# Performance work log

Measured on AMD Instinct MI355X. Metric: run time of the kernel, lower is better.

## Reference

```python
import jax, jax.numpy as jnp
import numpy as np

D_MODEL = 512
NUM_HEADS = 8
HEAD_DIM = D_MODEL // NUM_HEADS
ATTN_WINDOW = 256


def setup_inputs() -> dict:
    key = jax.random.key(0)
    ks = jax.random.split(key, 5)
    B, S = 2, 4096
    x = jax.random.normal(ks[0], (B, S, D_MODEL), dtype=jnp.float32)
    s = 1.0 / np.sqrt(D_MODEL)
    qkv_w = jax.random.uniform(ks[1], (3 * D_MODEL, D_MODEL), minval=-s, maxval=s, dtype=jnp.float32)
    qkv_b = jax.random.uniform(ks[2], (3 * D_MODEL,), minval=-s, maxval=s, dtype=jnp.float32)
    out_w = jax.random.uniform(ks[3], (D_MODEL, D_MODEL), minval=-s, maxval=s, dtype=jnp.float32)
    out_b = jax.random.uniform(ks[4], (D_MODEL,), minval=-s, maxval=s, dtype=jnp.float32)
    return {"x": x, "qkv_w": qkv_w, "qkv_b": qkv_b, "out_w": out_w, "out_b": out_b}


def reference(x, qkv_w, qkv_b, out_w, out_b):
    B, S, D = x.shape
    scale = HEAD_DIM ** (-0.5)
    qkv = x @ qkv_w.T + qkv_b                       # [B,S,3D]
    qkv = qkv.reshape(B, S, 3, NUM_HEADS, HEAD_DIM)
    q, k, v = qkv[:, :, 0], qkv[:, :, 1], qkv[:, :, 2]
    scores = jnp.einsum('bthd,bshd->bhts', q, k) * scale  # [B,H,S,S]
    i = jnp.arange(S)[:, None]
    j = jnp.arange(S)[None, :]
    # causal AND within sliding window of size ATTN_WINDOW
    mask = (j <= i) & (j >= i - ATTN_WINDOW)        # [S,S] bool
    scores = jnp.where(mask, scores, -jnp.inf)
    weights = jax.nn.softmax(scores, axis=-1)
    out = jnp.einsum('bhts,bshd->bthd', weights, v).reshape(B, S, D)
    return out @ out_w.T + out_b
```

## Files before the change

kernel.cpp:

```cpp
#include <hip/hip_runtime.h>

#define S_LEN 4096
#define BATCH 2
#define DM 512
#define NH 8
#define DH 64
#define WINDOW 256

typedef __bf16 bf16x8 __attribute__((ext_vector_type(8)));
typedef float f32x4 __attribute__((ext_vector_type(4)));

typedef const __attribute__((address_space(1))) unsigned int* gas_ptr;
typedef __attribute__((address_space(3))) unsigned int* las_ptr;

#define SCALE_LOG2E 0.1803368801111204f
#define FIXED_MAX 16.0f

#define BAR()                                   \
  do {                                          \
    asm volatile("" ::: "memory");              \
    __builtin_amdgcn_s_barrier();               \
    asm volatile("" ::: "memory");              \
  } while (0)
#define WAITVM(N) asm volatile("s_waitcnt vmcnt(" #N ")" ::: "memory")

__device__ __forceinline__ unsigned short b16(float f) {
  __bf16 h = (__bf16)f;
  return __builtin_bit_cast(unsigned short, h);
}

#define N4_X (8192 * 512 / 4)
#define N4_QW (1536 * 512 / 4)
#define N4_OW (512 * 512 / 4)
__global__ __launch_bounds__(256) void convert_all(const float* __restrict__ x,
                                                   const float* __restrict__ qw,
                                                   const float* __restrict__ ow,
                                                   unsigned short* __restrict__ dst) {
  const int i = blockIdx.x * blockDim.x + threadIdx.x;
  const float4* src;
  int off;
  if (i < N4_X) { src = (const float4*)x; off = 0; }
  else if (i < N4_X + N4_QW) { src = (const float4*)qw; off = N4_X; }
  else { src = (const float4*)ow; off = N4_X + N4_QW; }
  const float4 v = src[i - off];
  ushort4 o;
  o.x = b16(v.x); o.y = b16(v.y); o.z = b16(v.z); o.w = b16(v.w);
  ((ushort4*)dst)[i] = o;
}


__device__ __forceinline__ void gemm_core(const unsigned short* __restrict__ A,
                                          const unsigned short* __restrict__ Bm,
                                          int m0, int n0,
                                          unsigned short* sA, unsigned short* sB,
                                          f32x4 acc[4][4]) {
  const int t = threadIdx.x;
  const int wave = t >> 6, lane = t & 63;
  const int wr = wave >> 1, wc = wave & 1;
  const int quad = lane >> 4, l16 = lane & 15;
  const int sw2 = (l16 >> 1) & 3;
  const int cq = (quad ^ sw2) * 8;

#define QKV_STAGE(k0, buf)                                                       \
  do {                                                                           \
    _Pragma("unroll") for (int p = 0; p < 2; ++p) {                              \
      const int ci = wave * 128 + p * 64 + lane;               \
      const int row = ci >> 2;                                                   \
      const int cg = (ci & 3) ^ ((ci >> 3) & 3);  \
      const unsigned short* ga = A + (size_t)(m0 + row) * 512 + (k0) + cg * 8;   \
      __builtin_amdgcn_global_load_lds(                                          \
          (gas_ptr)(const void*)ga,                                              \
          (las_ptr)(void*)(sA + (buf) * 4096 + wave * 1024 + p * 512), 16, 0, 0);\
      const unsigned short* gb = Bm + (size_t)(n0 + row) * 512 + (k0) + cg * 8;  \
      __builtin_amdgcn_global_load_lds(                                          \
          (gas_ptr)(const void*)gb,                                              \
          (las_ptr)(void*)(sB + (buf) * 4096 + wave * 1024 + p * 512), 16, 0, 0);\
    }                                                                            \
  } while (0)

  QKV_STAGE(0, 0);
  for (int k0 = 0; k0 < 512; k0 += 32) {
    const int cur = (k0 >> 5) & 1;
    BAR();
    if (k0 + 32 < 512) {
      QKV_STAGE(k0 + 32, cur ^ 1);
      WAITVM(4);
    } else {
      WAITVM(0);
    }
    BAR();
    const unsigned short* bA = sA + cur * 4096;
    const unsigned short* bB = sB + cur * 4096;
    bf16x8 af[4], bff[4];
#pragma unroll
    for (int i = 0; i < 4; ++i)
      af[i] = *(const bf16x8*)&bA[(wr * 64 + i * 16 + l16) * 32 + cq];
#pragma unroll
    for (int j = 0; j < 4; ++j)
      bff[j] = *(const bf16x8*)&bB[(wc * 64 + j * 16 + l16) * 32 + cq];
#pragma unroll
    for (int i = 0; i < 4; ++i)
#pragma unroll
      for (int j = 0; j < 4; ++j)
        acc[i][j] = __builtin_amdgcn_mfma_f32_16x16x32_bf16(af[i], bff[j], acc[i][j], 0, 0, 0);
  }
#undef QKV_STAGE
}

__global__ __launch_bounds__(256, 4) void gemm_qkv(const unsigned short* __restrict__ xb,
                                                   const unsigned short* __restrict__ wb,
                                                   const float* __restrict__ bias,
                                                   unsigned short* __restrict__ Qb,
                                                   unsigned short* __restrict__ Kb,
                                                   unsigned short* __restrict__ Vt) {
  __shared__ __align__(16) unsigned short sA[2 * 128 * 32];
  __shared__ __align__(16) unsigned short sB[2 * 128 * 32];
  f32x4 acc[4][4] = {};
  const int id = blockIdx.x;
  const int X = id & 7;
  const int t2 = id >> 3;
  const int cb = t2 % 12;
  const int rb = (t2 / 12) * 8 + X;
  const int m0 = rb * 128, n0 = cb * 128;
  gemm_core(xb, wb, m0, n0, sA, sB, acc);

  const int t = threadIdx.x;
  const int wave = t >> 6, lane = t & 63;
  const int wr = wave >> 1, wc = wave & 1;
  const int quad = lane >> 4, l16 = lane & 15;
#pragma unroll
  for (int j = 0; j < 4; ++j) {
    const int n = n0 + wc * 64 + j * 16 + l16;
    const float bv = bias[n];
#pragma unroll
    for (int i = 0; i < 4; ++i) {
      const int mr = m0 + wr * 64 + i * 16 + quad * 4;
      if (n < DM) {
#pragma unroll
        for (int r = 0; r < 4; ++r)
          Qb[(size_t)(mr + r) * DM + n] = b16((acc[i][j][r] + bv) * SCALE_LOG2E);
      } else if (n < 2 * DM) {
#pragma unroll
        for (int r = 0; r < 4; ++r)
          Kb[(size_t)(mr + r) * DM + (n - DM)] = b16(acc[i][j][r] + bv);
      } else {
        const int d = n & 63, h = (n - 2 * DM) >> 6;
#pragma unroll
        for (int r = 0; r < 4; ++r) {
          const int m = mr + r;
          const int b = m >> 12, s = m & (S_LEN - 1);
          Vt[((size_t)((b * NH + h) * DH + d)) * S_LEN + s] = b16(acc[i][j][r] + bv);
        }
      }
    }
  }
}

__global__ __launch_bounds__(256) void gemm_out(const unsigned short* __restrict__ Ab,
                                                const unsigned short* __restrict__ wb,
                                                const float* __restrict__ bias,
                                                float* __restrict__ C) {
  __shared__ __align__(16) unsigned short sA[2 * 64 * 32];
  __shared__ __align__(16) unsigned short sB[2 * 128 * 32];
  const int t = threadIdx.x;
  const int wave = t >> 6, lane = t & 63;
  const int wr = wave >> 1, wc = wave & 1;
  const int quad = lane >> 4, l16 = lane & 15;
  const int sw2 = (l16 >> 1) & 3;
  const int cq = (quad ^ sw2) * 8;
  const int id = blockIdx.x;
  const int X = id & 7;
  const int t2 = id >> 3;
  const int cb = t2 % 4;
  const int rb = (t2 / 4) * 8 + X;
  const int m0 = rb * 64, n0 = cb * 128;

#define OUT_STAGE(k0, buf)                                                       \
  do {                                                                           \
    {                                                                            \
      const int row = t >> 2;                                                    \
      const int cg = (t & 3) ^ ((t >> 3) & 3);                                   \
      const unsigned short* ga = Ab + (size_t)(m0 + row) * 512 + (k0) + cg * 8;  \
      __builtin_amdgcn_global_load_lds(                                          \
          (gas_ptr)(const void*)ga,                                              \
          (las_ptr)(void*)(sA + (buf) * 2048 + wave * 512), 16, 0, 0);           \
    }                                                                            \
    _Pragma("unroll") for (int p = 0; p < 2; ++p) {                              \
      const int ci = wave * 128 + p * 64 + lane;                                 \
      const int row = ci >> 2;                                                   \
      const int cg = (ci & 3) ^ ((ci >> 3) & 3);                                 \
      const unsigned short* gb = wb + (size_t)(n0 + row) * 512 + (k0) + cg * 8;  \
      __builtin_amdgcn_global_load_lds(                                          \
          (gas_ptr)(const void*)gb,                                              \
          (las_ptr)(void*)(sB + (buf) * 4096 + wave * 1024 + p * 512), 16, 0, 0);\
    }                                                                            \
  } while (0)

  f32x4 acc[2][4] = {};
  OUT_STAGE(0, 0);
  for (int k0 = 0; k0 < 512; k0 += 32) {
    const int cur = (k0 >> 5) & 1;
    BAR();
    if (k0 + 32 < 512) {
      OUT_STAGE(k0 + 32, cur ^ 1);
      WAITVM(3);
    } else {
      WAITVM(0);
    }
    BAR();
    const unsigned short* bA = sA + cur * 2048;
    const unsigned short* bB = sB + cur * 4096;
    bf16x8 af[2], bff[4];
#pragma unroll
    for (int i = 0; i < 2; ++i)
      af[i] = *(const bf16x8*)&bA[(wr * 32 + i * 16 + l16) * 32 + cq];
#pragma unroll
    for (int j = 0; j < 4; ++j)
      bff[j] = *(const bf16x8*)&bB[(wc * 64 + j * 16 + l16) * 32 + cq];
#pragma unroll
    for (int i = 0; i < 2; ++i)
#pragma unroll
      for (int j = 0; j < 4; ++j)
        acc[i][j] = __builtin_amdgcn_mfma_f32_16x16x32_bf16(af[i], bff[j], acc[i][j], 0, 0, 0);
  }
#undef OUT_STAGE

#pragma unroll
  for (int j = 0; j < 4; ++j) {
    const int n = n0 + wc * 64 + j * 16 + l16;
    const float bv = bias[n];
#pragma unroll
    for (int i = 0; i < 2; ++i) {
      const int mr = m0 + wr * 32 + i * 16 + quad * 4;
#pragma unroll
      for (int r = 0; r < 4; ++r)
        C[(size_t)(mr + r) * DM + n] = acc[i][j][r] + bv;
    }
  }
}

__global__ __launch_bounds__(256) void attn_mfma(const unsigned short* __restrict__ Qb,
                                                 const unsigned short* __restrict__ Kb,
                                                 const unsigned short* __restrict__ Vt,
                                                 unsigned short* __restrict__ AO) {
  __shared__ __align__(16) unsigned short Ks[2 * 64 * 64];
  __shared__ __align__(16) unsigned short Vs[2 * 64 * 64];
  __shared__ __align__(16) unsigned short Ps[64 * 64];
  const int t = threadIdx.x;
  const int wave = t >> 6, lane = t & 63;
  const int quad = lane >> 4, l16 = lane & 15;

  const int id = blockIdx.x;
  const int X = id & 7;
  const int o = (id >> 3) & 7;
  const int h = (id >> 6) & 7;
  const int b = id >> 9;
  const int g = (X - h) & 7;
  const int qt = g * 8 + o;
  const int q0 = qt * 64;

  const unsigned short* Kbase = Kb + (size_t)b * S_LEN * DM + h * DH;
  const unsigned short* Vbase = Vt + (size_t)((b * NH + h) * DH) * S_LEN;

  const unsigned short* qrow =
      Qb + (size_t)(b * S_LEN + q0 + wave * 16 + l16) * DM + h * DH;
  const bf16x8 aq0 = *(const bf16x8*)(qrow + quad * 8);
  const bf16x8 aq1 = *(const bf16x8*)(qrow + 32 + quad * 8);

  const int first = (qt >= 4) ? 0 : (4 - qt);

  int grow[2], gcol[2];
#pragma unroll
  for (int s = 0; s < 2; ++s) {
    const int L = t + 256 * s;
    grow[s] = L >> 3;
    gcol[s] = ((L & 7) ^ (grow[s] & 7)) * 8;
  }

#define ATTN_STAGE(c0, buf)                                                       \
  do {                                                                            \
    _Pragma("unroll") for (int s = 0; s < 2; ++s) {                               \
      const unsigned short* gk = Kbase + (size_t)((c0) + grow[s]) * DM + gcol[s]; \
      __builtin_amdgcn_global_load_lds(                                           \
          (gas_ptr)(const void*)gk,                                               \
          (las_ptr)(void*)(Ks + (buf) * 4096 + wave * 512 + s * 2048), 16, 0, 0); \
      const unsigned short* gv = Vbase + (size_t)grow[s] * S_LEN + (c0) + gcol[s];\
      __builtin_amdgcn_global_load_lds(                                           \
          (gas_ptr)(const void*)gv,                                               \
          (las_ptr)(void*)(Vs + (buf) * 4096 + wave * 512 + s * 2048), 16, 0, 0); \
    }                                                                             \
  } while (0)

  ATTN_STAGE(q0 - WINDOW + first * 64, first & 1);

  float l_ = 0.f;
  f32x4 O[4] = {};

  const int sw = l16 & 7;
  const int c0q = (quad ^ sw) * 8;
  const int c1q = ((quad | 4) ^ sw) * 8;

#pragma unroll
  for (int c = 0; c < 5; ++c) {
    if (c < first) continue;
    const int c0 = q0 - WINDOW + c * 64;
    const int cur = c & 1;
    BAR();
    if (c < 4) {
      ATTN_STAGE(c0 + 64, cur ^ 1);
      WAITVM(4);
    } else {
      WAITVM(0);
    }
    BAR();

    const unsigned short* Kc = Ks + cur * 4096;
    const unsigned short* Vc = Vs + cur * 4096;

    f32x4 sc[4];
#pragma unroll
    for (int nt = 0; nt < 4; ++nt) {
      const int krow = (nt * 16 + l16) * 64;
      bf16x8 bk0 = *(const bf16x8*)&Kc[krow + c0q];
      bf16x8 bk1 = *(const bf16x8*)&Kc[krow + c1q];
      f32x4 z = {};
      z = __builtin_amdgcn_mfma_f32_16x16x32_bf16(bk0, aq0, z, 0, 0, 0);
      sc[nt] = __builtin_amdgcn_mfma_f32_16x16x32_bf16(bk1, aq1, z, 0, 0, 0);
    }

    const int iiq = wave * 16 + l16;
    const int prow = iiq * 64;
#pragma unroll
    for (int nt = 0; nt < 4; ++nt) {
#pragma unroll
      for (int r = 0; r < 4; ++r) {
        const int jjk = nt * 16 + quad * 4 + r;
        float p = exp2f(sc[nt][r] - FIXED_MAX);
        if (c == 0) p = (jjk >= iiq) ? p : 0.f;
        if (c == 4) p = (jjk <= iiq) ? p : 0.f;
        sc[nt][r] = p;
        l_ += p;
      }
      ushort4 pk;
      pk.x = b16(sc[nt][0]);
      pk.y = b16(sc[nt][1]);
      pk.z = b16(sc[nt][2]);
      pk.w = b16(sc[nt][3]);
      *(ushort4*)&Ps[prow + (((nt * 2 + (quad >> 1)) ^ sw) * 8) + (quad & 1) * 4] = pk;
    }

    const bf16x8 bp0 = *(const bf16x8*)&Ps[prow + c0q];
    const bf16x8 bp1 = *(const bf16x8*)&Ps[prow + c1q];

#pragma unroll
    for (int nt = 0; nt < 4; ++nt) {
      const int vrow = (nt * 16 + l16) * 64;
      bf16x8 bv0 = *(const bf16x8*)&Vc[vrow + c0q];
      bf16x8 bv1 = *(const bf16x8*)&Vc[vrow + c1q];
      O[nt] = __builtin_amdgcn_mfma_f32_16x16x32_bf16(bv0, bp0, O[nt], 0, 0, 0);
      O[nt] = __builtin_amdgcn_mfma_f32_16x16x32_bf16(bv1, bp1, O[nt], 0, 0, 0);
    }
  }
#undef ATTN_STAGE

  l_ += __shfl_xor(l_, 16);
  l_ += __shfl_xor(l_, 32);
  const float linv = 1.f / l_;

  unsigned short* aoRow =
      AO + (size_t)(b * S_LEN + q0 + wave * 16 + l16) * DM + h * DH;
#pragma unroll
  for (int nt = 0; nt < 4; ++nt) {
    ushort4 o4;
    o4.x = b16(O[nt][0] * linv);
    o4.y = b16(O[nt][1] * linv);
    o4.z = b16(O[nt][2] * linv);
    o4.w = b16(O[nt][3] * linv);
    *(ushort4*)(aoRow + nt * 16 + quad * 4) = o4;
  }
}

extern "C" void kernel_launch(void* const* d_in, const int* in_sizes, int n_in,
                              void* d_out, int out_size, void* d_ws, size_t ws_size,
                              hipStream_t stream) {
  const float* x = (const float*)d_in[0];
  const float* qkv_w = (const float*)d_in[1];
  const float* qkv_b = (const float*)d_in[2];
  const float* out_w = (const float*)d_in[3];
  const float* out_b = (const float*)d_in[4];
  float* out = (float*)d_out;

  const int M = BATCH * S_LEN;
  unsigned short* ws = (unsigned short*)d_ws;
  unsigned short* xb   = ws;
  unsigned short* wqkv = xb + (size_t)M * DM;
  unsigned short* wout = wqkv + 3 * DM * DM;
  unsigned short* Qb   = wout + DM * DM;
  unsigned short* Kb   = Qb + (size_t)M * DM;
  unsigned short* Vt   = Kb + (size_t)M * DM;
  unsigned short* AO   = Vt + (size_t)M * DM;

  convert_all<<<(N4_X + N4_QW + N4_OW) / 256, 256, 0, stream>>>(x, qkv_w, out_w, xb);

  gemm_qkv<<<768, 256, 0, stream>>>(xb, wqkv, qkv_b, Qb, Kb, Vt);

  attn_mfma<<<1024, 256, 0, stream>>>(Qb, Kb, Vt, AO);

  gemm_out<<<512, 256, 0, stream>>>(AO, wout, out_b, out);
}
```

Baseline: 127.7 us.

## Fuse fp32-to-bf16 conversion into GEMM staging, drop separate convert kernel

Removes the standalone conversion kernel and has the QKV and output GEMMs load fp32 inputs and weights into registers, convert them to bf16 and write them into swizzled LDS, with a register-prefetch double buffer. This saves one launch and the write and re-read of the bf16 copies of x and the weights. In exchange, each GEMM block now reads fp32 (twice the bytes) and re-converts the weights many times across tiles. Direct global-to-LDS loads are replaced by register staging, which adds VGPR pressure, and the launch-bounds occupancy hint on gemm_qkv is dropped.

```diff
diff --git a/kernel.cpp b/kernel.cpp
--- a/kernel.cpp
+++ b/kernel.cpp
@@ -9,6 +9,7 @@
 
 typedef __bf16 bf16x8 __attribute__((ext_vector_type(8)));
 typedef float f32x4 __attribute__((ext_vector_type(4)));
+typedef unsigned short u16x8 __attribute__((ext_vector_type(8)));
 
 typedef const __attribute__((address_space(1))) unsigned int* gas_ptr;
 typedef __attribute__((address_space(3))) unsigned int* las_ptr;
@@ -23,96 +24,27 @@
     asm volatile("" ::: "memory");              \
   } while (0)
 #define WAITVM(N) asm volatile("s_waitcnt vmcnt(" #N ")" ::: "memory")
+#define WAITLGKM(N) asm volatile("s_waitcnt lgkmcnt(" #N ")" ::: "memory")
 
 __device__ __forceinline__ unsigned short b16(float f) {
   __bf16 h = (__bf16)f;
   return __builtin_bit_cast(unsigned short, h);
 }
 
-#define N4_X (8192 * 512 / 4)
-#define N4_QW (1536 * 512 / 4)
-#define N4_OW (512 * 512 / 4)
-__global__ __launch_bounds__(256) void convert_all(const float* __restrict__ x,
-                                                   const float* __restrict__ qw,
-                                                   const float* __restrict__ ow,
-                                                   unsigned short* __restrict__ dst) {
-  const int i = blockIdx.x * blockDim.x + threadIdx.x;
-  const float4* src;
-  int off;
-  if (i < N4_X) { src = (const float4*)x; off = 0; }
-  else if (i < N4_X + N4_QW) { src = (const float4*)qw; off = N4_X; }
-  else { src = (const float4*)ow; off = N4_X + N4_QW; }
-  const float4 v = src[i - off];
-  ushort4 o;
-  o.x = b16(v.x); o.y = b16(v.y); o.z = b16(v.z); o.w = b16(v.w);
-  ((ushort4*)dst)[i] = o;
-}
-
-
-__device__ __forceinline__ void gemm_core(const unsigned short* __restrict__ A,
-                                          const unsigned short* __restrict__ Bm,
-                                          int m0, int n0,
-                                          unsigned short* sA, unsigned short* sB,
-                                          f32x4 acc[4][4]) {
-  const int t = threadIdx.x;
-  const int wave = t >> 6, lane = t & 63;
-  const int wr = wave >> 1, wc = wave & 1;
-  const int quad = lane >> 4, l16 = lane & 15;
-  const int sw2 = (l16 >> 1) & 3;
-  const int cq = (quad ^ sw2) * 8;
-
-#define QKV_STAGE(k0, buf)                                                       \
-  do {                                                                           \
-    _Pragma("unroll") for (int p = 0; p < 2; ++p) {                              \
-      const int ci = wave * 128 + p * 64 + lane;               \
-      const int row = ci >> 2;                                                   \
-      const int cg = (ci & 3) ^ ((ci >> 3) & 3);  \
-      const unsigned short* ga = A + (size_t)(m0 + row) * 512 + (k0) + cg * 8;   \
-      __builtin_amdgcn_global_load_lds(                                          \
-          (gas_ptr)(const void*)ga,                                              \
-          (las_ptr)(void*)(sA + (buf) * 4096 + wave * 1024 + p * 512), 16, 0, 0);\
-      const unsigned short* gb = Bm + (size_t)(n0 + row) * 512 + (k0) + cg * 8;  \
-      __builtin_amdgcn_global_load_lds(                                          \
-          (gas_ptr)(const void*)gb,                                              \
-          (las_ptr)(void*)(sB + (buf) * 4096 + wave * 1024 + p * 512), 16, 0, 0);\
-    }                                                                            \
-  } while (0)
-
-  QKV_STAGE(0, 0);
-  for (int k0 = 0; k0 < 512; k0 += 32) {
-    const int cur = (k0 >> 5) & 1;
-    BAR();
-    if (k0 + 32 < 512) {
-      QKV_STAGE(k0 + 32, cur ^ 1);
-      WAITVM(4);
-    } else {
-      WAITVM(0);
-    }
-    BAR();
-    const unsigned short* bA = sA + cur * 4096;
-    const unsigned short* bB = sB + cur * 4096;
-    bf16x8 af[4], bff[4];
-#pragma unroll
-    for (int i = 0; i < 4; ++i)
-      af[i] = *(const bf16x8*)&bA[(wr * 64 + i * 16 + l16) * 32 + cq];
-#pragma unroll
-    for (int j = 0; j < 4; ++j)
-      bff[j] = *(const bf16x8*)&bB[(wc * 64 + j * 16 + l16) * 32 + cq];
-#pragma unroll
-    for (int i = 0; i < 4; ++i)
-#pragma unroll
-      for (int j = 0; j < 4; ++j)
-        acc[i][j] = __builtin_amdgcn_mfma_f32_16x16x32_bf16(af[i], bff[j], acc[i][j], 0, 0, 0);
-  }
-#undef QKV_STAGE
-}
-
-__global__ __launch_bounds__(256, 4) void gemm_qkv(const unsigned short* __restrict__ xb,
-                                                   const unsigned short* __restrict__ wb,
-                                                   const float* __restrict__ bias,
-                                                   unsigned short* __restrict__ Qb,
-                                                   unsigned short* __restrict__ Kb,
-                                                   unsigned short* __restrict__ Vt) {
+__device__ __forceinline__ u16x8 pack8(float4 a, float4 b) {
+  u16x8 r;
+  r[0] = b16(a.x); r[1] = b16(a.y); r[2] = b16(a.z); r[3] = b16(a.w);
+  r[4] = b16(b.x); r[5] = b16(b.y); r[6] = b16(b.z); r[7] = b16(b.w);
+  return r;
+}
+
+
+__global__ __launch_bounds__(256) void gemm_qkv(const float* __restrict__ x,
+                                                const float* __restrict__ qw,
+                                                const float* __restrict__ bias,
+                                                unsigned short* __restrict__ Qb,
+                                                unsigned short* __restrict__ Kb,
+                                                unsigned short* __restrict__ Vt) {
   __shared__ __align__(16) unsigned short sA[2 * 128 * 32];
   __shared__ __align__(16) unsigned short sB[2 * 128 * 32];
   f32x4 acc[4][4] = {};
@@ -122,12 +54,67 @@
   const int cb = t2 % 12;
   const int rb = (t2 / 12) * 8 + X;
   const int m0 = rb * 128, n0 = cb * 128;
-  gemm_core(xb, wb, m0, n0, sA, sB, acc);
 
   const int t = threadIdx.x;
   const int wave = t >> 6, lane = t & 63;
   const int wr = wave >> 1, wc = wave & 1;
   const int quad = lane >> 4, l16 = lane & 15;
+  const int sw2 = (l16 >> 1) & 3;
+  const int cq = (quad ^ sw2) * 8;
+
+  const int srow = t >> 1, shalf = t & 1;
+  const int ssw = (srow >> 1) & 3;
+  const int slot0 = ((shalf * 2) ^ ssw) * 8;
+  const int slot1 = ((shalf * 2 + 1) ^ ssw) * 8;
+  const float* ax = x + (size_t)(m0 + srow) * 512 + shalf * 16;
+  const float* bx = qw + (size_t)(n0 + srow) * 512 + shalf * 16;
+
+  float4 ra[4], rbv[4];
+#define LOADREGS(k0)                                                    \
+  do {                                                                  \
+    const float* pa = ax + (k0);                                        \
+    ra[0] = *(const float4*)(pa + 0);  ra[1] = *(const float4*)(pa + 4);\
+    ra[2] = *(const float4*)(pa + 8);  ra[3] = *(const float4*)(pa + 12);\
+    const float* pb = bx + (k0);                                        \
+    rbv[0] = *(const float4*)(pb + 0); rbv[1] = *(const float4*)(pb + 4);\
+    rbv[2] = *(const float4*)(pb + 8); rbv[3] = *(const float4*)(pb + 12);\
+  } while (0)
+#define WRITEREGS(buf)                                                  \
+  do {                                                                  \
+    unsigned short* wA = sA + (buf) * 4096 + srow * 32;                 \
+    *(u16x8*)(wA + slot0) = pack8(ra[0], ra[1]);                        \
+    *(u16x8*)(wA + slot1) = pack8(ra[2], ra[3]);                        \
+    unsigned short* wB = sB + (buf) * 4096 + srow * 32;                 \
+    *(u16x8*)(wB + slot0) = pack8(rbv[0], rbv[1]);                      \
+    *(u16x8*)(wB + slot1) = pack8(rbv[2], rbv[3]);                      \
+  } while (0)
+
+  LOADREGS(0);
+  WRITEREGS(0);
+  for (int k = 0; k < 16; ++k) {
+    const int cur = k & 1;
+    if (k < 15) LOADREGS(k * 32 + 32);
+    WAITLGKM(0);
+    BAR();
+    const unsigned short* bA = sA + cur * 4096;
+    const unsigned short* bB = sB + cur * 4096;
+    bf16x8 af[4], bff[4];
+#pragma unroll
+    for (int i = 0; i < 4; ++i)
+      af[i] = *(const bf16x8*)&bA[(wr * 64 + i * 16 + l16) * 32 + cq];
+#pragma unroll
+    for (int j = 0; j < 4; ++j)
+      bff[j] = *(const bf16x8*)&bB[(wc * 64 + j * 16 + l16) * 32 + cq];
+#pragma unroll
+    for (int i = 0; i < 4; ++i)
+#pragma unroll
+      for (int j = 0; j < 4; ++j)
+        acc[i][j] = __builtin_amdgcn_mfma_f32_16x16x32_bf16(af[i], bff[j], acc[i][j], 0, 0, 0);
+    if (k < 15) WRITEREGS(cur ^ 1);
+  }
+#undef LOADREGS
+#undef WRITEREGS
+
 #pragma unroll
   for (int j = 0; j < 4; ++j) {
     const int n = n0 + wc * 64 + j * 16 + l16;
@@ -157,7 +144,7 @@
 }
 
 __global__ __launch_bounds__(256) void gemm_out(const unsigned short* __restrict__ Ab,
-                                                const unsigned short* __restrict__ wb,
+                                                const float* __restrict__ wb,
                                                 const float* __restrict__ bias,
                                                 float* __restrict__ C) {
   __shared__ __align__(16) unsigned short sA[2 * 64 * 32];
@@ -175,39 +162,41 @@
   const int rb = (t2 / 4) * 8 + X;
   const int m0 = rb * 64, n0 = cb * 128;
 
-#define OUT_STAGE(k0, buf)                                                       \
-  do {                                                                           \
-    {                                                                            \
-      const int row = t >> 2;                                                    \
-      const int cg = (t & 3) ^ ((t >> 3) & 3);                                   \
-      const unsigned short* ga = Ab + (size_t)(m0 + row) * 512 + (k0) + cg * 8;  \
-      __builtin_amdgcn_global_load_lds(                                          \
-          (gas_ptr)(const void*)ga,                                              \
-          (las_ptr)(void*)(sA + (buf) * 2048 + wave * 512), 16, 0, 0);           \
-    }                                                                            \
-    _Pragma("unroll") for (int p = 0; p < 2; ++p) {                              \
-      const int ci = wave * 128 + p * 64 + lane;                                 \
-      const int row = ci >> 2;                                                   \
-      const int cg = (ci & 3) ^ ((ci >> 3) & 3);                                 \
-      const unsigned short* gb = wb + (size_t)(n0 + row) * 512 + (k0) + cg * 8;  \
-      __builtin_amdgcn_global_load_lds(                                          \
-          (gas_ptr)(const void*)gb,                                              \
-          (las_ptr)(void*)(sB + (buf) * 4096 + wave * 1024 + p * 512), 16, 0, 0);\
-    }                                                                            \
+  const int srow = t >> 1, shalf = t & 1;
+  const int ssw = (srow >> 1) & 3;
+  const int slot0 = ((shalf * 2) ^ ssw) * 8;
+  const int slot1 = ((shalf * 2 + 1) ^ ssw) * 8;
+  const float* bx = wb + (size_t)(n0 + srow) * 512 + shalf * 16;
+  const int arow = t >> 2;
+  const int acg = (t & 3) ^ ((t >> 3) & 3);
+  const unsigned short* abase = Ab + (size_t)(m0 + arow) * 512 + acg * 8;
+
+  float4 rbv[4];
+#define OUT_LOAD(k0, buf)                                               \
+  do {                                                                  \
+    __builtin_amdgcn_global_load_lds(                                   \
+        (gas_ptr)(const void*)(abase + (k0)),                           \
+        (las_ptr)(void*)(sA + (buf) * 2048 + wave * 512), 16, 0, 0);    \
+    const float* pb = bx + (k0);                                        \
+    rbv[0] = *(const float4*)(pb + 0); rbv[1] = *(const float4*)(pb + 4);\
+    rbv[2] = *(const float4*)(pb + 8); rbv[3] = *(const float4*)(pb + 12);\
+  } while (0)
+#define OUT_WRITE(buf)                                                  \
+  do {                                                                  \
+    unsigned short* wB = sB + (buf) * 4096 + srow * 32;                 \
+    *(u16x8*)(wB + slot0) = pack8(rbv[0], rbv[1]);                      \
+    *(u16x8*)(wB + slot1) = pack8(rbv[2], rbv[3]);                      \
   } while (0)
 
   f32x4 acc[2][4] = {};
-  OUT_STAGE(0, 0);
-  for (int k0 = 0; k0 < 512; k0 += 32) {
-    const int cur = (k0 >> 5) & 1;
+  OUT_LOAD(0, 0);
+  WAITVM(0);
+  OUT_WRITE(0);
+  for (int k = 0; k < 16; ++k) {
+    const int cur = k & 1;
+    WAITLGKM(0);
     BAR();
-    if (k0 + 32 < 512) {
-      OUT_STAGE(k0 + 32, cur ^ 1);
-      WAITVM(3);
-    } else {
-      WAITVM(0);
-    }
-    BAR();
+    if (k < 15) OUT_LOAD(k * 32 + 32, cur ^ 1);
     const unsigned short* bA = sA + cur * 2048;
     const unsigned short* bB = sB + cur * 4096;
     bf16x8 af[2], bff[4];
@@ -222,8 +211,13 @@
 #pragma unroll
       for (int j = 0; j < 4; ++j)
         acc[i][j] = __builtin_amdgcn_mfma_f32_16x16x32_bf16(af[i], bff[j], acc[i][j], 0, 0, 0);
-  }
-#undef OUT_STAGE
+    if (k < 15) {
+      WAITVM(0);
+      OUT_WRITE(cur ^ 1);
+    }
+  }
+#undef OUT_LOAD
+#undef OUT_WRITE
 
 #pragma unroll
   for (int j = 0; j < 4; ++j) {
@@ -392,19 +386,14 @@
 
   const int M = BATCH * S_LEN;
   unsigned short* ws = (unsigned short*)d_ws;
-  unsigned short* xb   = ws;
-  unsigned short* wqkv = xb + (size_t)M * DM;
-  unsigned short* wout = wqkv + 3 * DM * DM;
-  unsigned short* Qb   = wout + DM * DM;
-  unsigned short* Kb   = Qb + (size_t)M * DM;
-  unsigned short* Vt   = Kb + (size_t)M * DM;
-  unsigned short* AO   = Vt + (size_t)M * DM;
-
-  convert_all<<<(N4_X + N4_QW + N4_OW) / 256, 256, 0, stream>>>(x, qkv_w, out_w, xb);
-
-  gemm_qkv<<<768, 256, 0, stream>>>(xb, wqkv, qkv_b, Qb, Kb, Vt);
+  unsigned short* Qb = ws;
+  unsigned short* Kb = Qb + (size_t)M * DM;
+  unsigned short* Vt = Kb + (size_t)M * DM;
+  unsigned short* AO = Vt + (size_t)M * DM;
+
+  gemm_qkv<<<768, 256, 0, stream>>>(x, qkv_w, qkv_b, Qb, Kb, Vt);
 
   attn_mfma<<<1024, 256, 0, stream>>>(Qb, Kb, Vt, AO);
 
-  gemm_out<<<512, 256, 0, stream>>>(AO, wout, out_b, out);
-}
+  gemm_out<<<512, 256, 0, stream>>>(AO, out_w, out_b, out);
+}
```

Measured after the change: 164.6 us. 28.9% more time.
